# Kernel optimization log

Hardware: AMD Instinct MI355X
Metric: run time of the kernel (lower is better)

## Reference

```python
import jax, jax.numpy as jnp
import numpy as np
import math

B, T, H, NH, BLOCK = 2, 2048, 1024, 16, 2048
HS = H // NH  # 64, even as required by RoPE


def make_rope_cache(hs, block):
    # positions t = 1..block (note: source starts at 1, not 0)
    t = np.arange(1, block + 1, dtype=np.float32)[:, None]          # (block, 1)
    i = np.arange(1, hs // 2 + 1, dtype=np.float32)[None, :]        # (1, hs/2)
    theta = (1.0 / 10000.0) ** (2.0 * (i - 1.0) / hs)               # (1, hs/2)
    ang = t * theta                                                  # (block, hs/2)
    return jnp.asarray(np.stack([np.cos(ang), np.sin(ang)], axis=-1))  # (block, hs/2, 2)


def setup_inputs() -> dict:
    key = jax.random.key(0)
    ks = jax.random.split(key, 10)
    s = 0.02
    x = jax.random.normal(ks[0], (B, T, H), jnp.float32)
    masks = jax.random.randint(ks[1], (B, T), 0, 2, jnp.int32)  # 1 = padding token
    Wq = jax.random.normal(ks[2], (H, H), jnp.float32) * s
    bq = jnp.zeros((H,), jnp.float32)
    Wk = jax.random.normal(ks[3], (H, H), jnp.float32) * s
    bk = jnp.zeros((H,), jnp.float32)
    Wv = jax.random.normal(ks[4], (H, H), jnp.float32) * s
    bv = jnp.zeros((H,), jnp.float32)
    Wo = jax.random.normal(ks[5], (H, H), jnp.float32) * s  # final_proj, no bias
    rope = make_rope_cache(HS, BLOCK)
    return {"x": x, "masks": masks, "Wq": Wq, "bq": bq, "Wk": Wk, "bk": bk,
            "Wv": Wv, "bv": bv, "Wo": Wo, "rope": rope}


def _apply_rope(x, cos, sin):
    # x: (B, nh, T, hs); cos/sin: (T, hs/2) broadcast over (B, nh)
    xe, xo = x[..., ::2], x[..., 1::2]
    real = cos * xe - sin * xo
    imag = sin * xe + cos * xo
    return jnp.stack([real, imag], axis=-1).reshape(x.shape)


def reference(x, masks, Wq, bq, Wk, bk, Wv, bv, Wo, rope):
    Bn, Tn, Hn = x.shape
    nh, hs = NH, Hn // NH

    def proj(W, b):
        # torch Linear: x @ W.T + b -> (B, nh, T, hs)
        return (x @ W.T + b).reshape(Bn, Tn, nh, hs).transpose(0, 2, 1, 3)

    Q, K, V = proj(Wq, bq), proj(Wk, bk), proj(Wv, bv)
    cos, sin = rope[:Tn, :, 0], rope[:Tn, :, 1]
    Q = _apply_rope(Q, cos, sin)
    K = _apply_rope(K, cos, sin)

    att = jnp.einsum('bhqd,bhkd->bhqk', Q, K) * (1.0 / math.sqrt(hs))
    causal = jnp.tril(jnp.ones((Tn, Tn), bool))
    att = jnp.where(causal[None, None, :, :], att, -1e10)          # causal mask
    att = jnp.where((masks == 1)[:, None, None, :], -1e10, att)   # padding mask on keys
    att = jax.nn.softmax(att, axis=-1)

    y = jnp.einsum('bhqk,bhkd->bhqd', att, V)
    y = y.transpose(0, 2, 1, 3).reshape(Bn, Tn, Hn)
    return y @ Wo.T  # final_proj has no bias
```

## Files before the change

kernel.cpp:

```cpp
#include <hip/hip_runtime.h>

typedef short short8 __attribute__((ext_vector_type(8)));
typedef float floatx4 __attribute__((ext_vector_type(4)));
typedef unsigned short u16;
typedef unsigned long long u64;

#define Tn 2048
#define Kdim 1024
#define QSCALE 0.18033688011112042f
#define FIXEDMAX 20.0f

__device__ inline u16 f2bf(float x) {
    union { float f; unsigned u; } c; c.f = x;
    unsigned u = c.u;
    u += 0x7fffu + ((u >> 16) & 1u);
    return (u16)(u >> 16);
}
__device__ inline float bf2f(u16 h) {
    union { unsigned u; float f; } c; c.u = ((unsigned)h) << 16;
    return c.f;
}
__device__ inline floatx4 mfma16(short8 a, short8 b, floatx4 c) {
    return __builtin_amdgcn_mfma_f32_16x16x32_bf16(a, b, c, 0, 0, 0);
}
__device__ inline void async16(const void* g, void* l) {
    __builtin_amdgcn_global_load_lds((const __attribute__((address_space(1))) void*)g,
                                     (__attribute__((address_space(3))) void*)l, 16, 0, 0);
}

__global__ __launch_bounds__(256) void cvt_all_k(
    const float* __restrict__ x, const float* __restrict__ wq, const float* __restrict__ wk,
    const float* __restrict__ wv, const float* __restrict__ wo, u16* __restrict__ dst)
{
    int i = blockIdx.x * 256 + threadIdx.x;
    const float* s; int off;
    if (i < 1048576) { s = x; off = i; }
    else {
        int j = i - 1048576; int seg = j >> 18; off = j & 262143;
        s = (seg == 0) ? wq : (seg == 1) ? wk : (seg == 2) ? wv : wo;
    }
    float4 v = ((const float4*)s)[off];
    u64 pk = (u64)f2bf(v.x) | ((u64)f2bf(v.y) << 16) | ((u64)f2bf(v.z) << 32) | ((u64)f2bf(v.w) << 48);
    ((u64*)dst)[i] = pk;
}

__global__ __launch_bounds__(256, 5) void gemm_qkv_k(
    const u16* __restrict__ A,
    const u16* __restrict__ W0, const u16* __restrict__ W1, const u16* __restrict__ W2,
    const float* __restrict__ b0, const float* __restrict__ b1, const float* __restrict__ b2,
    u16* o0, u16* o1, u16* o2,
    const float2* __restrict__ rope)
{
    int z = blockIdx.z;
    const u16* W = (z == 0) ? W0 : (z == 1 ? W1 : W2);
    const float* bias = (z == 0) ? b0 : (z == 1 ? b1 : b2);
    u16* outp = (z == 0) ? o0 : (z == 1 ? o1 : o2);

    __shared__ __align__(16) char lds[24576];
    int tid = threadIdx.x;
    int w = tid >> 6, lane = tid & 63, quad = lane >> 4, l15 = lane & 15;
    int m0 = blockIdx.y * 128, n0 = blockIdx.x * 64;
    int wm = w * 32;

    floatx4 acc[2][4];
    floatx4 vzero = {0.f, 0.f, 0.f, 0.f};
#pragma unroll
    for (int i = 0; i < 2; ++i)
#pragma unroll
        for (int j = 0; j < 4; ++j) acc[i][j] = vzero;

    for (int k0 = 0; k0 < Kdim; k0 += 64) {
#pragma unroll
        for (int j = 0; j < 4; ++j) {
            int f = j * 256 + tid, r = f >> 3, c = (f & 7) ^ (r & 7);
            async16(A + (size_t)(m0 + r) * Kdim + k0 + c * 8, lds + j * 4096 + w * 1024);
        }
#pragma unroll
        for (int j = 0; j < 2; ++j) {
            int f = j * 256 + tid, r = f >> 3, c = (f & 7) ^ (r & 7);
            async16(W + (size_t)(n0 + r) * Kdim + k0 + c * 8, lds + 16384 + j * 4096 + w * 1024);
        }
        __syncthreads();
        short8 af[2][2];
#pragma unroll
        for (int mt = 0; mt < 2; ++mt) {
            int ra = wm + mt * 16 + l15;
            const char* pa = lds + ra * 128;
#pragma unroll
            for (int ks = 0; ks < 2; ++ks)
                af[mt][ks] = *(const short8*)(pa + (((ks * 4 + quad) ^ (ra & 7)) << 4));
        }
#pragma unroll
        for (int ks = 0; ks < 2; ++ks)
#pragma unroll
            for (int nt = 0; nt < 4; ++nt) {
                int rb = nt * 16 + l15;
                short8 bf = *(const short8*)(lds + 16384 + rb * 128 + (((ks * 4 + quad) ^ (rb & 7)) << 4));
                acc[0][nt] = mfma16(af[0][ks], bf, acc[0][nt]);
                acc[1][nt] = mfma16(af[1][ks], bf, acc[1][nt]);
            }
        __syncthreads();
    }

    int mbase = m0 + wm;
    if (z <= 1) {
        float osc = (z == 0) ? QSCALE : 1.0f;
#pragma unroll
        for (int nt = 0; nt < 4; ++nt) {
            int col = n0 + nt * 16 + l15;
            float bv = bias[col];
            int p = (col & 63) >> 1;
#pragma unroll
            for (int mt = 0; mt < 2; ++mt) {
                floatx4 a = acc[mt][nt];
#pragma unroll
                for (int r = 0; r < 4; ++r) {
                    int row = mbase + mt * 16 + quad * 4 + r;
                    float v = a[r] + bv;
                    float ov = __shfl_xor(v, 1, 64);
                    float2 cs = rope[(row & (Tn - 1)) * 32 + p];
                    float res = (cs.x * v + ((lane & 1) ? cs.y * ov : -cs.y * ov)) * osc;
                    float pres = __shfl_xor(res, 1, 64);
                    if (!(lane & 1)) {
                        unsigned pk = (unsigned)f2bf(res) | ((unsigned)f2bf(pres) << 16);
                        *(unsigned*)(outp + (size_t)row * 1024 + col) = pk;
                    }
                }
            }
        }
    } else {
#pragma unroll
        for (int nt = 0; nt < 4; ++nt) {
            int col = n0 + nt * 16 + l15;
            float bv = bias[col];
#pragma unroll
            for (int mt = 0; mt < 2; ++mt) {
                floatx4 a = acc[mt][nt];
                int row0 = mbase + mt * 16 + quad * 4;
                int bb = row0 >> 11, t0 = row0 & (Tn - 1);
                u64 pk = (u64)f2bf(a[0] + bv) | ((u64)f2bf(a[1] + bv) << 16)
                       | ((u64)f2bf(a[2] + bv) << 32) | ((u64)f2bf(a[3] + bv) << 48);
                *(u64*)(outp + (size_t)(bb * 1024 + col) * Tn + t0) = pk;
            }
        }
    }
}

__global__ __launch_bounds__(256, 4) void gemm_o_k(
    const u16* __restrict__ A, const u16* __restrict__ W, float* __restrict__ out)
{
    __shared__ __align__(16) char lds[16384];
    int tid = threadIdx.x;
    int w = tid >> 6, lane = tid & 63, quad = lane >> 4, l15 = lane & 15;
    int m0 = blockIdx.y * 64, n0 = blockIdx.x * 64;
    int wm = (w >> 1) * 32, wn = (w & 1) * 32;

    floatx4 acc[2][2];
    floatx4 vzero = {0.f, 0.f, 0.f, 0.f};
#pragma unroll
    for (int i = 0; i < 2; ++i)
#pragma unroll
        for (int j = 0; j < 2; ++j) acc[i][j] = vzero;

    for (int k0 = 0; k0 < Kdim; k0 += 64) {
#pragma unroll
        for (int j = 0; j < 2; ++j) {
            int f = j * 256 + tid, r = f >> 3, c = (f & 7) ^ (r & 7);
            async16(A + (size_t)(m0 + r) * Kdim + k0 + c * 8, lds + j * 4096 + w * 1024);
            async16(W + (size_t)(n0 + r) * Kdim + k0 + c * 8, lds + 8192 + j * 4096 + w * 1024);
        }
        __syncthreads();
        short8 af[2][2];
#pragma unroll
        for (int mt = 0; mt < 2; ++mt) {
            int ra = wm + mt * 16 + l15;
            const char* pa = lds + ra * 128;
#pragma unroll
            for (int ks = 0; ks < 2; ++ks)
                af[mt][ks] = *(const short8*)(pa + (((ks * 4 + quad) ^ (ra & 7)) << 4));
        }
#pragma unroll
        for (int ks = 0; ks < 2; ++ks)
#pragma unroll
            for (int nt = 0; nt < 2; ++nt) {
                int rb = wn + nt * 16 + l15;
                short8 bf = *(const short8*)(lds + 8192 + rb * 128 + (((ks * 4 + quad) ^ (rb & 7)) << 4));
                acc[0][nt] = mfma16(af[0][ks], bf, acc[0][nt]);
                acc[1][nt] = mfma16(af[1][ks], bf, acc[1][nt]);
            }
        __syncthreads();
    }

#pragma unroll
    for (int nt = 0; nt < 2; ++nt) {
        int col = n0 + wn + nt * 16 + l15;
#pragma unroll
        for (int mt = 0; mt < 2; ++mt) {
            floatx4 a = acc[mt][nt];
#pragma unroll
            for (int r = 0; r < 4; ++r) {
                int row = m0 + wm + mt * 16 + quad * 4 + r;
                out[(size_t)row * 1024 + col] = a[r];
            }
        }
    }
}

__global__ __launch_bounds__(64) void vmean_k(const u16* __restrict__ Vt, float* __restrict__ vmean) {
    int row = blockIdx.x;
    int lane = threadIdx.x;
    const u16* p = Vt + (size_t)row * Tn;
    float s = 0.f;
    for (int i = lane * 8; i < Tn; i += 512) {
        short8 v = *(const short8*)(p + i);
#pragma unroll
        for (int j = 0; j < 8; ++j) s += bf2f((u16)v[j]);
    }
#pragma unroll
    for (int off = 1; off < 64; off <<= 1) s += __shfl_xor(s, off, 64);
    if (lane == 0) vmean[row] = s * (1.f / 2048.f);
}

__global__ __launch_bounds__(256) void flash_k(
    const u16* __restrict__ Qb, const u16* __restrict__ Kb, const u16* __restrict__ Vt,
    const int* __restrict__ masks, const float* __restrict__ vmean, u16* __restrict__ Yb)
{
    int bh = blockIdx.y;
    int b = bh >> 4, h = bh & 15;
    int tid = threadIdx.x, w = tid >> 6, lane = tid & 63, quad = lane >> 4, l15 = lane & 15;
    int sc = (lane & 7) ^ (lane >> 3);

    __shared__ __align__(16) u16 ldsK[2][64 * 64];
    __shared__ __align__(16) u16 ldsV[2][64 * 64];
    __shared__ __align__(16) u16 ldsP[4][16 * 72];
    __shared__ u64 smsk[32];

#pragma unroll
    for (int j = 0; j < 8; ++j) {
        u64 mk = __ballot(masks[b * Tn + (w * 8 + j) * 64 + lane] != 0);
        if (lane == 0) smsk[w * 8 + j] = mk;
    }

    auto stage = [&](int bb, int k0) {
#pragma unroll
        for (int j = 0; j < 2; ++j) {
            int row = j * 32 + w * 8 + (lane >> 3);
            const u16* gk = Kb + (size_t)(b * Tn + k0 + row) * 1024 + h * 64 + sc * 8;
            async16(gk, (char*)&ldsK[bb][0] + (j * 32 + w * 8) * 128);
            const u16* gv = Vt + (size_t)(b * 1024 + h * 64 + row) * Tn + k0 + sc * 8;
            async16(gv, (char*)&ldsV[bb][0] + (j * 32 + w * 8) * 128);
        }
    };
    floatx4 vzero = {0.f, 0.f, 0.f, 0.f};

    for (int ph = 0; ph < 2; ++ph) {
        int qt = ph ? blockIdx.x : (31 - blockIdx.x);
        int q0 = qt * 64 + w * 16;

        short8 qf[2];
        {
            const u16* qp = Qb + (size_t)(b * Tn + q0 + l15) * 1024 + h * 64 + quad * 8;
            qf[0] = *(const short8*)qp;
            qf[1] = *(const short8*)(qp + 32);
        }
        floatx4 o[4];
        float lsum[4] = {0.f, 0.f, 0.f, 0.f};
#pragma unroll
        for (int i = 0; i < 4; ++i) o[i] = vzero;

        int ktiles = qt + 1;
        stage(0, 0);
        for (int kt = 0; kt < ktiles; ++kt) {
            int k0 = kt * 64;
            int bb = kt & 1;
            __syncthreads();

            short8 kf[4][2], vf[4][2];
#pragma unroll
            for (int f = 0; f < 4; ++f) {
                int key = f * 16 + l15;
                const char* kbase = (const char*)&ldsK[bb][0] + key * 128;
                const char* vbase = (const char*)&ldsV[bb][0] + key * 128;
#pragma unroll
                for (int ks = 0; ks < 2; ++ks) {
                    int slot = ((quad + ks * 4) ^ (key & 7)) << 4;
                    kf[f][ks] = *(const short8*)(kbase + slot);
                    vf[f][ks] = *(const short8*)(vbase + slot);
                }
            }
            if (kt + 1 < ktiles) stage(bb ^ 1, k0 + 64);

            floatx4 s[4];
#pragma unroll
            for (int f = 0; f < 4; ++f) {
                s[f] = mfma16(qf[0], kf[f][0], vzero);
                s[f] = mfma16(qf[1], kf[f][1], s[f]);
            }

            u64 msk = smsk[kt];
            unsigned mlo = (unsigned)msk, mhi = (unsigned)(msk >> 32);
            int mb[4];
            mb[0] = (mlo >> l15) & 1; mb[1] = (mlo >> (l15 + 16)) & 1;
            mb[2] = (mhi >> l15) & 1; mb[3] = (mhi >> (l15 + 16)) & 1;

#pragma unroll
            for (int r = 0; r < 4; ++r) {
                int lim = q0 + quad * 4 + r - k0;
                float psum = 0.f;
#pragma unroll
                for (int f = 0; f < 4; ++f) {
                    float v = (16 * f + l15 > lim || mb[f]) ? -1e10f : s[f][r];
                    float p = __builtin_amdgcn_exp2f(v - FIXEDMAX);
                    psum += p;
                    unsigned u = __float_as_uint(p) + 0x8000u;
                    ldsP[w][(quad * 4 + r) * 72 + f * 16 + l15] = (u16)(u >> 16);
                }
                lsum[r] += psum;
            }
            __asm__ volatile("s_waitcnt lgkmcnt(0)" ::: "memory");
            short8 pf0 = *(const short8*)((const char*)&ldsP[w][0] + l15 * 144 + quad * 16);
            short8 pf1 = *(const short8*)((const char*)&ldsP[w][0] + l15 * 144 + 64 + quad * 16);
#pragma unroll
            for (int nb = 0; nb < 4; ++nb) {
                o[nb] = mfma16(pf0, vf[nb][0], o[nb]);
                o[nb] = mfma16(pf1, vf[nb][1], o[nb]);
            }
        }
        __syncthreads();

#pragma unroll
        for (int r = 0; r < 4; ++r) {
            int qq = q0 + quad * 4 + r;
            float l = lsum[r];
#pragma unroll
            for (int off = 1; off < 16; off <<= 1) l += __shfl_xor(l, off, 64);
            bool degen = (l == 0.f);
            float linv = 1.0f / l;
#pragma unroll
            for (int nb = 0; nb < 4; ++nb) {
                int d = nb * 16 + l15;
                float val = degen ? vmean[b * 1024 + h * 64 + d] : o[nb][r] * linv;
                float pv = __shfl_xor(val, 1, 64);
                if (!(lane & 1)) {
                    unsigned pk = (unsigned)f2bf(val) | ((unsigned)f2bf(pv) << 16);
                    *(unsigned*)(Yb + (size_t)(b * Tn + qq) * 1024 + h * 64 + d) = pk;
                }
            }
        }
    }
}

extern "C" void kernel_launch(void* const* d_in, const int* in_sizes, int n_in,
                              void* d_out, int out_size, void* d_ws, size_t ws_size,
                              hipStream_t stream) {
    const float* x  = (const float*)d_in[0];
    const int* masks = (const int*)d_in[1];
    const float* Wq = (const float*)d_in[2];
    const float* bq = (const float*)d_in[3];
    const float* Wk = (const float*)d_in[4];
    const float* bk = (const float*)d_in[5];
    const float* Wv = (const float*)d_in[6];
    const float* bv = (const float*)d_in[7];
    const float* Wo = (const float*)d_in[8];
    const float2* rope = (const float2*)d_in[9];
    float* out = (float*)d_out;

    char* ws = (char*)d_ws;
    u16* xb   = (u16*)(ws);
    u16* Wqb  = (u16*)(ws + (8  << 20));
    u16* Wkb  = (u16*)(ws + (10 << 20));
    u16* Wvb  = (u16*)(ws + (12 << 20));
    u16* Wob  = (u16*)(ws + (14 << 20));
    u16* Qb   = (u16*)(ws + (16 << 20));
    u16* Kb2  = (u16*)(ws + (24 << 20));
    u16* Vt   = (u16*)(ws + (32 << 20));
    u16* Yb   = (u16*)(ws + (40 << 20));
    float* vm = (float*)(ws + (48 << 20));

    cvt_all_k<<<8192, 256, 0, stream>>>(x, Wq, Wk, Wv, Wo, xb);

    gemm_qkv_k<<<dim3(16, 32, 3), 256, 0, stream>>>(xb, Wqb, Wkb, Wvb, bq, bk, bv,
                                                    Qb, Kb2, Vt, rope);
    vmean_k<<<2048, 64, 0, stream>>>(Vt, vm);
    flash_k<<<dim3(16, 32), 256, 0, stream>>>(Qb, Kb2, Vt, masks, vm, Yb);
    gemm_o_k<<<dim3(16, 64), 256, 0, stream>>>(Yb, Wob, out);
}
```

Baseline: 202.3 us.

## Launch one flash block per query tile with XCD-aware ordering and mask fast path

Replaces the paired-tile scheme (each block handling two query tiles, 512 blocks) with one query tile per block on a 1D grid of 1024, ordered largest tile first and with head/batch interleaved so neighbouring blocks spread across XCDs. Key-padding masks are now kept in registers and fetched by shuffle rather than through shared memory. Tiles that lie fully below the diagonal skip the causal comparison. The P scratch drops its padding and uses an XOR-swizzled layout instead. More blocks with uneven lengths could lower occupancy balance; the odd self-assignment ldsP[w][0]=ldsP[w][0] adds a stray LDS access.

Measured after the change: 193.6 us. -4.3%, faster.

```diff
diff --git a/kernel.cpp b/kernel.cpp
--- a/kernel.cpp
+++ b/kernel.cpp
@@ -225,20 +225,22 @@
     const u16* __restrict__ Qb, const u16* __restrict__ Kb, const u16* __restrict__ Vt,
     const int* __restrict__ masks, const float* __restrict__ vmean, u16* __restrict__ Yb)
 {
-    int bh = blockIdx.y;
+    int bid = blockIdx.x;
+    int bh = (bid & 7) * 4 + ((bid >> 3) & 3);
+    int qt = 31 - (bid >> 5);
     int b = bh >> 4, h = bh & 15;
     int tid = threadIdx.x, w = tid >> 6, lane = tid & 63, quad = lane >> 4, l15 = lane & 15;
     int sc = (lane & 7) ^ (lane >> 3);
 
     __shared__ __align__(16) u16 ldsK[2][64 * 64];
     __shared__ __align__(16) u16 ldsV[2][64 * 64];
-    __shared__ __align__(16) u16 ldsP[4][16 * 72];
-    __shared__ u64 smsk[32];
-
-#pragma unroll
-    for (int j = 0; j < 8; ++j) {
-        u64 mk = __ballot(masks[b * Tn + (w * 8 + j) * 64 + lane] != 0);
-        if (lane == 0) smsk[w * 8 + j] = mk;
+    __shared__ __align__(16) u16 ldsP[4][16 * 64];
+
+    int ktiles = qt + 1;
+    unsigned blo = 0, bhi = 0;
+    for (int j = 0; j < ktiles; ++j) {
+        u64 mk = __ballot(masks[b * Tn + j * 64 + lane] != 0);
+        if (lane == j) { blo = (unsigned)mk; bhi = (unsigned)(mk >> 32); }
     }
 
     auto stage = [&](int bb, int k0) {
@@ -253,56 +255,69 @@
     };
     floatx4 vzero = {0.f, 0.f, 0.f, 0.f};
 
-    for (int ph = 0; ph < 2; ++ph) {
-        int qt = ph ? blockIdx.x : (31 - blockIdx.x);
-        int q0 = qt * 64 + w * 16;
-
-        short8 qf[2];
-        {
-            const u16* qp = Qb + (size_t)(b * Tn + q0 + l15) * 1024 + h * 64 + quad * 8;
-            qf[0] = *(const short8*)qp;
-            qf[1] = *(const short8*)(qp + 32);
-        }
-        floatx4 o[4];
-        float lsum[4] = {0.f, 0.f, 0.f, 0.f};
-#pragma unroll
-        for (int i = 0; i < 4; ++i) o[i] = vzero;
-
-        int ktiles = qt + 1;
-        stage(0, 0);
-        for (int kt = 0; kt < ktiles; ++kt) {
-            int k0 = kt * 64;
-            int bb = kt & 1;
-            __syncthreads();
-
-            short8 kf[4][2], vf[4][2];
-#pragma unroll
-            for (int f = 0; f < 4; ++f) {
-                int key = f * 16 + l15;
-                const char* kbase = (const char*)&ldsK[bb][0] + key * 128;
-                const char* vbase = (const char*)&ldsV[bb][0] + key * 128;
-#pragma unroll
-                for (int ks = 0; ks < 2; ++ks) {
-                    int slot = ((quad + ks * 4) ^ (key & 7)) << 4;
-                    kf[f][ks] = *(const short8*)(kbase + slot);
-                    vf[f][ks] = *(const short8*)(vbase + slot);
+    int q0 = qt * 64 + w * 16;
+    short8 qf[2];
+    {
+        const u16* qp = Qb + (size_t)(b * Tn + q0 + l15) * 1024 + h * 64 + quad * 8;
+        qf[0] = *(const short8*)qp;
+        qf[1] = *(const short8*)(qp + 32);
+    }
+    floatx4 o[4];
+    float lsum[4] = {0.f, 0.f, 0.f, 0.f};
+#pragma unroll
+    for (int i = 0; i < 4; ++i) o[i] = vzero;
+
+    stage(0, 0);
+    for (int kt = 0; kt < ktiles; ++kt) {
+        int k0 = kt * 64;
+        int bb = kt & 1;
+        __syncthreads();
+
+        short8 kf[4][2], vf[4][2];
+#pragma unroll
+        for (int f = 0; f < 4; ++f) {
+            int key = f * 16 + l15;
+            const char* kbase = (const char*)&ldsK[bb][0] + key * 128;
+            const char* vbase = (const char*)&ldsV[bb][0] + key * 128;
+#pragma unroll
+            for (int ks = 0; ks < 2; ++ks) {
+                int slot = ((quad + ks * 4) ^ (key & 7)) << 4;
+                kf[f][ks] = *(const short8*)(kbase + slot);
+                vf[f][ks] = *(const short8*)(vbase + slot);
+            }
+        }
+        if (kt + 1 < ktiles) stage(bb ^ 1, k0 + 64);
+
+        floatx4 s[4];
+#pragma unroll
+        for (int f = 0; f < 4; ++f) {
+            s[f] = mfma16(qf[0], kf[f][0], vzero);
+            s[f] = mfma16(qf[1], kf[f][1], s[f]);
+        }
+
+        unsigned mlo = __shfl(blo, kt, 64), mhi = __shfl(bhi, kt, 64);
+        int mb[4];
+        mb[0] = (mlo >> l15) & 1; mb[1] = (mlo >> (l15 + 16)) & 1;
+        mb[2] = (mhi >> l15) & 1; mb[3] = (mhi >> (l15 + 16)) & 1;
+
+        if (k0 + 63 <= q0) {
+#pragma unroll
+            for (int r = 0; r < 4; ++r) {
+                float psum = 0.f;
+#pragma unroll
+                for (int f = 0; f < 4; ++f) {
+                    float v = mb[f] ? -1e10f : s[f][r];
+                    float p = __builtin_amdgcn_exp2f(v - FIXEDMAX);
+                    psum += p;
+                    unsigned u = __float_as_uint(p) + 0x8000u;
+                    int row = quad * 4 + r, key = f * 16 + l15;
+                    ldsP[w][0] = ldsP[w][0];
+                    *((u16*)((char*)&ldsP[w][0] + row * 128 +
+                             ((((key >> 3) ^ (row & 7))) << 4) + (key & 7) * 2)) = (u16)(u >> 16);
                 }
-            }
-            if (kt + 1 < ktiles) stage(bb ^ 1, k0 + 64);
-
-            floatx4 s[4];
-#pragma unroll
-            for (int f = 0; f < 4; ++f) {
-                s[f] = mfma16(qf[0], kf[f][0], vzero);
-                s[f] = mfma16(qf[1], kf[f][1], s[f]);
-            }
-
-            u64 msk = smsk[kt];
-            unsigned mlo = (unsigned)msk, mhi = (unsigned)(msk >> 32);
-            int mb[4];
-            mb[0] = (mlo >> l15) & 1; mb[1] = (mlo >> (l15 + 16)) & 1;
-            mb[2] = (mhi >> l15) & 1; mb[3] = (mhi >> (l15 + 16)) & 1;
-
+                lsum[r] += psum;
+            }
+        } else {
 #pragma unroll
             for (int r = 0; r < 4; ++r) {
                 int lim = q0 + quad * 4 + r - k0;
@@ -313,38 +328,39 @@
                     float p = __builtin_amdgcn_exp2f(v - FIXEDMAX);
                     psum += p;
                     unsigned u = __float_as_uint(p) + 0x8000u;
-                    ldsP[w][(quad * 4 + r) * 72 + f * 16 + l15] = (u16)(u >> 16);
+                    int row = quad * 4 + r, key = f * 16 + l15;
+                    *((u16*)((char*)&ldsP[w][0] + row * 128 +
+                             ((((key >> 3) ^ (row & 7))) << 4) + (key & 7) * 2)) = (u16)(u >> 16);
                 }
                 lsum[r] += psum;
             }
-            __asm__ volatile("s_waitcnt lgkmcnt(0)" ::: "memory");
-            short8 pf0 = *(const short8*)((const char*)&ldsP[w][0] + l15 * 144 + quad * 16);
-            short8 pf1 = *(const short8*)((const char*)&ldsP[w][0] + l15 * 144 + 64 + quad * 16);
-#pragma unroll
-            for (int nb = 0; nb < 4; ++nb) {
-                o[nb] = mfma16(pf0, vf[nb][0], o[nb]);
-                o[nb] = mfma16(pf1, vf[nb][1], o[nb]);
-            }
-        }
-        __syncthreads();
-
-#pragma unroll
-        for (int r = 0; r < 4; ++r) {
-            int qq = q0 + quad * 4 + r;
-            float l = lsum[r];
-#pragma unroll
-            for (int off = 1; off < 16; off <<= 1) l += __shfl_xor(l, off, 64);
-            bool degen = (l == 0.f);
-            float linv = 1.0f / l;
-#pragma unroll
-            for (int nb = 0; nb < 4; ++nb) {
-                int d = nb * 16 + l15;
-                float val = degen ? vmean[b * 1024 + h * 64 + d] : o[nb][r] * linv;
-                float pv = __shfl_xor(val, 1, 64);
-                if (!(lane & 1)) {
-                    unsigned pk = (unsigned)f2bf(val) | ((unsigned)f2bf(pv) << 16);
-                    *(unsigned*)(Yb + (size_t)(b * Tn + qq) * 1024 + h * 64 + d) = pk;
-                }
+        }
+        __asm__ volatile("s_waitcnt lgkmcnt(0)" ::: "memory");
+        short8 pf0 = *(const short8*)((const char*)&ldsP[w][0] + l15 * 128 + ((quad ^ (l15 & 7)) << 4));
+        short8 pf1 = *(const short8*)((const char*)&ldsP[w][0] + l15 * 128 + (((quad + 4) ^ (l15 & 7)) << 4));
+#pragma unroll
+        for (int nb = 0; nb < 4; ++nb) {
+            o[nb] = mfma16(pf0, vf[nb][0], o[nb]);
+            o[nb] = mfma16(pf1, vf[nb][1], o[nb]);
+        }
+    }
+
+#pragma unroll
+    for (int r = 0; r < 4; ++r) {
+        int qq = q0 + quad * 4 + r;
+        float l = lsum[r];
+#pragma unroll
+        for (int off = 1; off < 16; off <<= 1) l += __shfl_xor(l, off, 64);
+        bool degen = (l == 0.f);
+        float linv = 1.0f / l;
+#pragma unroll
+        for (int nb = 0; nb < 4; ++nb) {
+            int d = nb * 16 + l15;
+            float val = degen ? vmean[b * 1024 + h * 64 + d] : o[nb][r] * linv;
+            float pv = __shfl_xor(val, 1, 64);
+            if (!(lane & 1)) {
+                unsigned pk = (unsigned)f2bf(val) | ((unsigned)f2bf(pv) << 16);
+                *(unsigned*)(Yb + (size_t)(b * Tn + qq) * 1024 + h * 64 + d) = pk;
             }
         }
     }
@@ -382,6 +398,6 @@
     gemm_qkv_k<<<dim3(16, 32, 3), 256, 0, stream>>>(xb, Wqb, Wkb, Wvb, bq, bk, bv,
                                                     Qb, Kb2, Vt, rope);
     vmean_k<<<2048, 64, 0, stream>>>(Vt, vm);
-    flash_k<<<dim3(16, 32), 256, 0, stream>>>(Qb, Kb2, Vt, masks, vm, Yb);
+    flash_k<<<1024, 256, 0, stream>>>(Qb, Kb2, Vt, masks, vm, Yb);
     gemm_o_k<<<dim3(16, 64), 256, 0, stream>>>(Yb, Wob, out);
 }
```
